# Kernel tuning notes

Measured on AMD Instinct MI355X. Metric: run time of the kernel, lower is better.

Reference implementation:

```python
import jax, jax.numpy as jnp
import numpy as np

N_FEATURES = 170
D_MODEL = 64
N_HEADS = 4
ALPHA = 0.1
LN_EPS = 1e-5
LEAKY_SLOPE = 0.01  # torch F.leaky_relu default
N = 3 * N_FEATURES  # 510
B = 32


def setup_inputs() -> dict:
    key = jax.random.key(0)
    ks = jax.random.split(key, 10)
    D, H = D_MODEL, N_HEADS
    s = 1.0 / np.sqrt(D)
    return {
        "x": jax.random.normal(ks[0], (B, N, D), dtype=jnp.float32),
        "causal_graph": jax.random.uniform(ks[1], (N, N), dtype=jnp.float32),
        # nn.Linear(d_model, d_model*n_heads, bias=False): stored here as (D, H*D) for x @ W
        "W": jax.random.uniform(ks[2], (D, H * D), jnp.float32, -s, s),
        "attention_w": jax.random.normal(ks[3], (H, 2 * D), dtype=jnp.float32),
        # Conv2d(2, n_heads, 3, padding=1): OIHW kernel
        "conv_w": jax.random.uniform(ks[4], (H, 2, 3, 3), jnp.float32, -1/np.sqrt(18), 1/np.sqrt(18)),
        "conv_b": jax.random.uniform(ks[5], (H,), jnp.float32, -1/np.sqrt(18), 1/np.sqrt(18)),
        # nn.Linear(d_model, 2*d_model): stored as (D, 2D)
        "fcg_w": jax.random.uniform(ks[6], (D, 2 * D), jnp.float32, -s, s),
        "fcg_b": jax.random.uniform(ks[7], (2 * D,), jnp.float32, -s, s),
        "ln_g": jnp.ones((D,), jnp.float32),
        "ln_b": jnp.zeros((D,), jnp.float32),
    }


def reference(x, causal_graph, W, attention_w, conv_w, conv_b, fcg_w, fcg_b, ln_g, ln_b):
    Bz, Nn, D = x.shape
    H = N_HEADS
    # shared projection: (B, N, H, D)
    xt = (x @ W).reshape(Bz, Nn, H, D)
    # GAT-style additive scores: concat-dot decomposed into two dot products
    w1, w2 = attention_w[:, :D], attention_w[:, D:]  # each (H, D)
    s_i = jnp.einsum('bnhd,hd->bhn', xt, w1)  # source term
    s_j = jnp.einsum('bnhd,hd->bhn', xt, w2)  # target term
    e = s_i[:, :, :, None] + s_j[:, :, None, :]  # (B, H, N, N)
    A_eva = jnp.where(e >= 0, e, LEAKY_SLOPE * e)  # leaky_relu
    # fuse mean attention with causal graph via 3x3 conv
    A_mean = A_eva.mean(axis=1)  # (B, N, N)
    causal = jnp.broadcast_to(causal_graph[None], (Bz, Nn, Nn))
    stacked = jnp.stack([A_mean, causal], axis=1)  # (B, 2, N, N)
    A_st = jax.lax.conv_general_dilated(
        stacked, conv_w, window_strides=(1, 1), padding=((1, 1), (1, 1)),
        dimension_numbers=('NCHW', 'OIHW', 'NCHW'))
    A_st = A_st + conv_b[None, :, None, None]  # (B, H, N, N)
    A = jax.nn.softmax(ALPHA * A_eva + (1.0 - ALPHA) * A_st, axis=-1)
    # multi-head aggregation then head-mean
    out = jnp.einsum('bhnm,bmhd->bnhd', A, xt).mean(axis=2)  # (B, N, D)
    # GLU
    g = out @ fcg_w + fcg_b  # (B, N, 2D)
    a, b = g[..., :D], g[..., D:]
    glu = a * jax.nn.sigmoid(b)
    # residual + layernorm
    y = glu + x
    mu = y.mean(axis=-1, keepdims=True)
    var = ((y - mu) ** 2).mean(axis=-1, keepdims=True)
    y = (y - mu) * jax.lax.rsqrt(var + LN_EPS) * ln_g + ln_b
    return y, A
```

## Files before the change

kernel.cpp:

```cpp
#include <hip/hip_runtime.h>

#define Bz 32
#define Nn 510
#define Dd 64
#define Hh 4
#define HD_ 256
#define Kpad 512
#define ALPHA_ 0.1f
#define LNEPS 1e-5f
#define SLOPE 0.01f
#define NEG_INF -3.0e38f

typedef __attribute__((ext_vector_type(8))) short short8;
typedef __attribute__((ext_vector_type(4))) float floatx4;

__device__ inline float wredsum(float v) {
  #pragma unroll
  for (int off = 32; off; off >>= 1) v += __shfl_xor(v, off, 64);
  return v;
}
__device__ inline float wredmax(float v) {
  #pragma unroll
  for (int off = 32; off; off >>= 1) v = fmaxf(v, __shfl_xor(v, off, 64));
  return v;
}
__device__ inline unsigned short f2bf(float f) {
  unsigned int u = __float_as_uint(f);
  unsigned int r = (u + 0x7fffu + ((u >> 16) & 1u)) >> 16;
  return (unsigned short)r;
}

__global__ __launch_bounds__(256) void k1_xt(const float* __restrict__ x,
                                             const float* __restrict__ W,
                                             const float* __restrict__ attw,
                                             unsigned short* __restrict__ xtT,
                                             float* __restrict__ si,
                                             float* __restrict__ sj) {
  __shared__ float Wl[64][68];
  __shared__ float xr[32][68];
  __shared__ unsigned short st[64 * 33];
  const int t = threadIdx.x;
  const int rt = blockIdx.x;
  const int b = blockIdx.y;
  const int ch = blockIdx.z;
  #pragma unroll
  for (int k = 0; k < 4; k++) {
    int f = t + k * 256;
    int kr = f >> 4;
    int c = (f & 15) * 4;
    *(float4*)&Wl[kr][c] = *(const float4*)&W[kr * HD_ + ch * 64 + c];
  }
  #pragma unroll
  for (int k = 0; k < 2; k++) {
    int f = t + k * 256;
    int r = f >> 4;
    int c = (f & 15) * 4;
    int row = rt * 32 + r;
    float4 v = make_float4(0.f, 0.f, 0.f, 0.f);
    if (row < Nn) v = *(const float4*)&x[(b * Nn + row) * Dd + c];
    *(float4*)&xr[r][c] = v;
  }
  __syncthreads();
  const int tg = t >> 4;
  const int tc = t & 15;
  const int rb = tg * 2, c0 = tc * 4;
  float acc[2][4] = {};
  #pragma unroll
  for (int k4 = 0; k4 < 16; k4++) {
    float4 xv0 = *(float4*)&xr[rb][k4 * 4];
    float4 xv1 = *(float4*)&xr[rb + 1][k4 * 4];
    #pragma unroll
    for (int kk = 0; kk < 4; kk++) {
      float4 wv = *(float4*)&Wl[k4 * 4 + kk][c0];
      float xs0 = (&xv0.x)[kk];
      float xs1 = (&xv1.x)[kk];
      acc[0][0] = fmaf(xs0, wv.x, acc[0][0]);
      acc[0][1] = fmaf(xs0, wv.y, acc[0][1]);
      acc[0][2] = fmaf(xs0, wv.z, acc[0][2]);
      acc[0][3] = fmaf(xs0, wv.w, acc[0][3]);
      acc[1][0] = fmaf(xs1, wv.x, acc[1][0]);
      acc[1][1] = fmaf(xs1, wv.y, acc[1][1]);
      acc[1][2] = fmaf(xs1, wv.z, acc[1][2]);
      acc[1][3] = fmaf(xs1, wv.w, acc[1][3]);
    }
  }
  #pragma unroll
  for (int cc = 0; cc < 4; cc++) {
    #pragma unroll
    for (int r = 0; r < 2; r++) {
      st[(c0 + cc) * 33 + rb + r] = f2bf(acc[r][cc]);
    }
  }
  float w1v[4], w2v[4];
  #pragma unroll
  for (int cc = 0; cc < 4; cc++) {
    w1v[cc] = attw[ch * 128 + c0 + cc];
    w2v[cc] = attw[ch * 128 + 64 + c0 + cc];
  }
  #pragma unroll
  for (int r = 0; r < 2; r++) {
    float p1 = acc[r][0] * w1v[0] + acc[r][1] * w1v[1] +
               acc[r][2] * w1v[2] + acc[r][3] * w1v[3];
    float p2 = acc[r][0] * w2v[0] + acc[r][1] * w2v[1] +
               acc[r][2] * w2v[2] + acc[r][3] * w2v[3];
    #pragma unroll
    for (int off = 1; off <= 8; off <<= 1) {
      p1 += __shfl_xor(p1, off, 64);
      p2 += __shfl_xor(p2, off, 64);
    }
    if (tc == 0) {
      int row = rt * 32 + rb + r;
      if (row < Nn) {
        si[(b * 4 + ch) * Nn + row] = p1;
        sj[(b * 4 + ch) * Nn + row] = p2;
      }
    }
  }
  __syncthreads();
  if (t < 64) {
    unsigned short* dst = &xtT[((size_t)(b * 4 + ch) * 64 + t) * Kpad + rt * 32];
    #pragma unroll
    for (int q = 0; q < 4; q++) {
      short8 v;
      #pragma unroll
      for (int k = 0; k < 8; k++) v[k] = (short)st[t * 33 + q * 8 + k];
      *(short8*)&dst[q * 8] = v;
    }
  }
}

__global__ __launch_bounds__(256) void k2a_cconv(const float* __restrict__ causal,
                                                 const float* __restrict__ convw,
                                                 const float* __restrict__ convb,
                                                 float* __restrict__ ccv) {
  const int i = blockIdx.x;
  const int t = threadIdx.x;
  #pragma unroll
  for (int qq = 0; qq < 2; qq++) {
    const int j = t + qq * 256;
    float tap[9];
    #pragma unroll
    for (int r3 = 0; r3 < 3; r3++) {
      int ii = i - 1 + r3;
      #pragma unroll
      for (int c3 = 0; c3 < 3; c3++) {
        int jj = j - 1 + c3;
        tap[r3 * 3 + c3] = (ii >= 0 && ii < Nn && jj >= 0 && jj < Nn)
                               ? causal[ii * Nn + jj] : 0.f;
      }
    }
    #pragma unroll
    for (int h = 0; h < 4; h++) {
      float acc = convb[h];
      #pragma unroll
      for (int q = 0; q < 9; q++) acc = fmaf(convw[h * 18 + 9 + q], tap[q], acc);
      ccv[((size_t)h * Nn + i) * 512 + j] = acc;
    }
  }
}

__global__ __launch_bounds__(256) void k2_attn(const float* __restrict__ si,
                                               const float* __restrict__ sj,
                                               const float* __restrict__ ccv,
                                               const float* __restrict__ convw,
                                               float* __restrict__ A) {
  __shared__ float am_t[10 * 8 * 68];
  __shared__ float sjl[4 * 8 * 68];
  __shared__ float sil[4][12];
  __shared__ float cwl[4][9];
  const int t = threadIdx.x;
  const int i0 = blockIdx.x * 8;
  const int b = blockIdx.y;
  if (t < 36) cwl[t / 9][t % 9] = convw[(t / 9) * 18 + (t % 9)];
  if (t < 40) {
    int h = t / 10, r = t % 10;
    int iq = i0 + r - 1;
    sil[h][r] = (iq >= 0 && iq < Nn) ? si[(b * 4 + h) * Nn + iq] : 0.f;
  }
  if (t >= 64 && t < 224) {
    int q = t - 64;
    int r = q >> 4, rem = q & 15;
    int e = rem >> 1, side = rem & 1;
    am_t[(r * 8 + e) * 68 + side * 65] = 0.f;
  }
  for (int f = t; f < 2048; f += 256) {
    int h = f >> 9, j = f & 511;
    float v = (j < Nn) ? sj[(b * 4 + h) * Nn + j] : 0.f;
    sjl[(h * 8 + (j & 7)) * 68 + (j >> 3) + 1] = v;
  }
  __syncthreads();
  for (int f = t; f < 5120; f += 256) {
    int r = f >> 9, j = f & 511;
    int iq = i0 + r - 1;
    float am = 0.f;
    if (iq >= 0 && iq < Nn && j < Nn) {
      float s = 0.f;
      #pragma unroll
      for (int h = 0; h < 4; h++) {
        float e2 = sil[h][r] + sjl[(h * 8 + (j & 7)) * 68 + (j >> 3) + 1];
        s += (e2 >= 0.f) ? e2 : SLOPE * e2;
      }
      am = 0.25f * s;
    }
    am_t[(r * 8 + (j & 7)) * 68 + (j >> 3) + 1] = am;
  }
  __syncthreads();
  const int w = t >> 6, L = t & 63;
  const int j0 = L * 8;
  #pragma unroll
  for (int qq = 0; qq < 2; qq++) {
    const int il = w * 2 + qq;
    const int i = i0 + il;
    if (i >= Nn) continue;
    float conv[4][8];
    #pragma unroll
    for (int h = 0; h < 4; h++) {
      const float* cp = &ccv[((size_t)h * Nn + i) * 512 + j0];
      float4 c0 = *(const float4*)&cp[0];
      float4 c1 = *(const float4*)&cp[4];
      conv[h][0] = c0.x; conv[h][1] = c0.y; conv[h][2] = c0.z; conv[h][3] = c0.w;
      conv[h][4] = c1.x; conv[h][5] = c1.y; conv[h][6] = c1.z; conv[h][7] = c1.w;
    }
    #pragma unroll
    for (int r3 = 0; r3 < 3; r3++) {
      const float* ba = &am_t[((il + r3) * 8) * 68];
      float a[10];
      a[0] = ba[7 * 68 + L];
      #pragma unroll
      for (int e = 0; e < 8; e++) a[1 + e] = ba[e * 68 + L + 1];
      a[9] = ba[0 * 68 + L + 2];
      #pragma unroll
      for (int h = 0; h < 4; h++) {
        float w0 = cwl[h][r3 * 3], w1 = cwl[h][r3 * 3 + 1], w2 = cwl[h][r3 * 3 + 2];
        #pragma unroll
        for (int e = 0; e < 8; e++) {
          float cv = conv[h][e];
          cv = fmaf(w0, a[e], cv);
          cv = fmaf(w1, a[e + 1], cv);
          cv = fmaf(w2, a[e + 2], cv);
          conv[h][e] = cv;
        }
      }
    }
    #pragma unroll
    for (int h = 0; h < 4; h++) {
      const float sih = sil[h][il + 1];
      float v[8];
      float mx = NEG_INF;
      #pragma unroll
      for (int e = 0; e < 8; e++) {
        float ee = sih + sjl[(h * 8 + e) * 68 + L + 1];
        float l = (ee >= 0.f) ? ee : SLOPE * ee;
        float val = ALPHA_ * l + (1.0f - ALPHA_) * conv[h][e];
        v[e] = (j0 + e < Nn) ? val : NEG_INF;
        mx = fmaxf(mx, v[e]);
      }
      mx = wredmax(mx);
      float p[8], s = 0.f;
      #pragma unroll
      for (int e = 0; e < 8; e++) {
        p[e] = __expf(v[e] - mx);
        s += p[e];
      }
      s = wredsum(s);
      const float inv = 1.f / s;
      #pragma unroll
      for (int e = 0; e < 8; e++) p[e] *= inv;
      float* Ar = &A[((size_t)(b * 4 + h) * Nn + i) * Nn + j0];
      *(float4*)&Ar[0] = make_float4(p[0], p[1], p[2], p[3]);
      if (L < 63) {
        *(float4*)&Ar[4] = make_float4(p[4], p[5], p[6], p[7]);
      } else {
        *(float2*)&Ar[4] = make_float2(p[4], p[5]);
      }
    }
  }
}

__global__ __launch_bounds__(256) void k3_out(const float* __restrict__ A,
                                              const unsigned short* __restrict__ xtT,
                                              const float* __restrict__ x,
                                              const float* __restrict__ fcgw,
                                              const float* __restrict__ fcgb,
                                              const float* __restrict__ lng,
                                              const float* __restrict__ lnb,
                                              float* __restrict__ y) {
  __shared__ unsigned short Asub[2][16 * 72];
  __shared__ float ol[16][64];
  __shared__ float gl[2][128];
  const int t = threadIdx.x;
  const int n0 = blockIdx.x * 16;
  const int b = blockIdx.y;
  const int w = t >> 6, L = t & 63;
  const int quad = L >> 4, l16 = L & 15;
  const int wc = w * 16;
  const int ar = t >> 4;
  const int amc = (t & 15) * 4;
  const int nrow = n0 + ar;
  floatx4 acc = {0.f, 0.f, 0.f, 0.f};

  auto stage = [&](int p) {
    const int h = p >> 3;
    const int m = (p & 7) * 64 + amc;
    float av[4] = {0.f, 0.f, 0.f, 0.f};
    if (nrow < Nn) {
      const float* src = &A[((size_t)(b * 4 + h) * Nn + nrow) * Nn + m];
      if (m + 3 < Nn) {
        float2 v0 = *(const float2*)&src[0];
        float2 v1 = *(const float2*)&src[2];
        av[0] = v0.x; av[1] = v0.y; av[2] = v1.x; av[3] = v1.y;
      } else {
        int lim = Nn - m;
        #pragma unroll
        for (int q = 0; q < 4; q++) if (q < lim) av[q] = src[q];
      }
    }
    ushort4 u;
    u.x = f2bf(av[0]); u.y = f2bf(av[1]);
    u.z = f2bf(av[2]); u.w = f2bf(av[3]);
    *(ushort4*)&Asub[p & 1][ar * 72 + amc] = u;
  };

  stage(0);
  __syncthreads();
  #pragma unroll 2
  for (int p = 0; p < 32; p++) {
    if (p + 1 < 32) stage(p + 1);
    const int h = p >> 3;
    const unsigned short* Xr =
        &xtT[((size_t)(b * 4 + h) * 64 + wc + l16) * Kpad + (p & 7) * 64];
    short8 af0 = *(short8*)&Asub[p & 1][l16 * 72 + quad * 8];
    short8 bf0 = *(const short8*)&Xr[quad * 8];
    acc = __builtin_amdgcn_mfma_f32_16x16x32_bf16(af0, bf0, acc, 0, 0, 0);
    short8 af1 = *(short8*)&Asub[p & 1][l16 * 72 + 32 + quad * 8];
    short8 bf1 = *(const short8*)&Xr[32 + quad * 8];
    acc = __builtin_amdgcn_mfma_f32_16x16x32_bf16(af1, bf1, acc, 0, 0, 0);
    __syncthreads();
  }

  #pragma unroll
  for (int reg = 0; reg < 4; reg++) {
    ol[quad * 4 + reg][wc + l16] = 0.25f * acc[reg];
  }
  __syncthreads();
  const int kk = t & 127;
  const int rg = t >> 7;
  for (int it = 0; it < 8; it++) {
    const int r = it * 2 + rg;
    const int row = n0 + r;
    float g = fcgb[kk];
    #pragma unroll
    for (int d = 0; d < 64; d++) g = fmaf(ol[r][d], fcgw[d * 128 + kk], g);
    gl[rg][kk] = g;
    __syncthreads();
    if (kk < 64 && row < Nn) {
      float a = gl[rg][kk];
      float bb = gl[rg][kk + 64];
      float glu = a / (1.f + __expf(-bb));
      float yv = glu + x[(b * Nn + row) * Dd + kk];
      float mu = wredsum(yv) * (1.f / 64.f);
      float dv = yv - mu;
      float var = wredsum(dv * dv) * (1.f / 64.f);
      float o = dv * rsqrtf(var + LNEPS) * lng[kk] + lnb[kk];
      y[(b * Nn + row) * Dd + kk] = o;
    }
    __syncthreads();
  }
}

extern "C" void kernel_launch(void* const* d_in, const int* in_sizes, int n_in,
                              void* d_out, int out_size, void* d_ws, size_t ws_size,
                              hipStream_t stream) {
  const float* x      = (const float*)d_in[0];
  const float* causal = (const float*)d_in[1];
  const float* W      = (const float*)d_in[2];
  const float* attw   = (const float*)d_in[3];
  const float* convw  = (const float*)d_in[4];
  const float* convb  = (const float*)d_in[5];
  const float* fcgw   = (const float*)d_in[6];
  const float* fcgb   = (const float*)d_in[7];
  const float* lng    = (const float*)d_in[8];
  const float* lnb    = (const float*)d_in[9];

  float* ws = (float*)d_ws;
  float* si = ws;
  float* sj = si + (size_t)Bz * Hh * Nn;
  unsigned short* xtT = (unsigned short*)(sj + (size_t)Bz * Hh * Nn + 16);
  float* ccv = (float*)(xtT + (size_t)Bz * Hh * Dd * Kpad);

  float* yout = (float*)d_out;
  float* Aout = yout + (size_t)Bz * Nn * Dd;

  k2a_cconv<<<dim3(Nn), 256, 0, stream>>>(causal, convw, convb, ccv);
  k1_xt  <<<dim3(16, Bz, 4), 256, 0, stream>>>(x, W, attw, xtT, si, sj);
  k2_attn<<<dim3(64, Bz), 256, 0, stream>>>(si, sj, ccv, convw, Aout);
  k3_out <<<dim3(32, Bz), 256, 0, stream>>>(Aout, xtT, x, fcgw, fcgb, lng, lnb, yout);
}
```

Before: 260.5 us.

## Compute attention-mean tile in registers with wave shuffles instead of LDS

The attention kernel no longer stages sj, si, conv weights and the mean-attention halo tile in shared memory behind two barriers. Each thread now loads its own sj and si values into registers and recomputes the leaky-relu head-mean for its three conv rows. Neighbouring columns for the 3x3 stencil come from wave shuffles. This removes LDS traffic and synchronisation, but adds redundant ALU work (mean rows recomputed per wave), more register pressure, and direct global reads of the conv weights.

```diff
diff --git a/kernel.cpp b/kernel.cpp
--- a/kernel.cpp
+++ b/kernel.cpp
@@ -164,94 +164,90 @@
                                                const float* __restrict__ ccv,
                                                const float* __restrict__ convw,
                                                float* __restrict__ A) {
-  __shared__ float am_t[10 * 8 * 68];
-  __shared__ float sjl[4 * 8 * 68];
-  __shared__ float sil[4][12];
-  __shared__ float cwl[4][9];
   const int t = threadIdx.x;
   const int i0 = blockIdx.x * 8;
   const int b = blockIdx.y;
-  if (t < 36) cwl[t / 9][t % 9] = convw[(t / 9) * 18 + (t % 9)];
-  if (t < 40) {
-    int h = t / 10, r = t % 10;
-    int iq = i0 + r - 1;
-    sil[h][r] = (iq >= 0 && iq < Nn) ? si[(b * 4 + h) * Nn + iq] : 0.f;
-  }
-  if (t >= 64 && t < 224) {
-    int q = t - 64;
-    int r = q >> 4, rem = q & 15;
-    int e = rem >> 1, side = rem & 1;
-    am_t[(r * 8 + e) * 68 + side * 65] = 0.f;
-  }
-  for (int f = t; f < 2048; f += 256) {
-    int h = f >> 9, j = f & 511;
-    float v = (j < Nn) ? sj[(b * 4 + h) * Nn + j] : 0.f;
-    sjl[(h * 8 + (j & 7)) * 68 + (j >> 3) + 1] = v;
-  }
-  __syncthreads();
-  for (int f = t; f < 5120; f += 256) {
-    int r = f >> 9, j = f & 511;
-    int iq = i0 + r - 1;
-    float am = 0.f;
-    if (iq >= 0 && iq < Nn && j < Nn) {
-      float s = 0.f;
-      #pragma unroll
-      for (int h = 0; h < 4; h++) {
-        float e2 = sil[h][r] + sjl[(h * 8 + (j & 7)) * 68 + (j >> 3) + 1];
-        s += (e2 >= 0.f) ? e2 : SLOPE * e2;
-      }
-      am = 0.25f * s;
-    }
-    am_t[(r * 8 + (j & 7)) * 68 + (j >> 3) + 1] = am;
-  }
-  __syncthreads();
   const int w = t >> 6, L = t & 63;
   const int j0 = L * 8;
+  float sjv[4][8];
+  #pragma unroll
+  for (int h = 0; h < 4; h++) {
+    const float* bp = &sj[(size_t)(b * 4 + h) * Nn];
+    if (j0 + 7 < Nn) {
+      #pragma unroll
+      for (int q = 0; q < 4; q++) {
+        float2 v = *(const float2*)&bp[j0 + q * 2];
+        sjv[h][q * 2] = v.x;
+        sjv[h][q * 2 + 1] = v.y;
+      }
+    } else {
+      #pragma unroll
+      for (int e = 0; e < 8; e++) sjv[h][e] = (j0 + e < Nn) ? bp[j0 + e] : 0.f;
+    }
+  }
+  float silr[4][4];
+  #pragma unroll
+  for (int rr = 0; rr < 4; rr++) {
+    int iq = i0 + w * 2 - 1 + rr;
+    bool ok = (iq >= 0 && iq < Nn);
+    #pragma unroll
+    for (int h = 0; h < 4; h++)
+      silr[h][rr] = ok ? si[(size_t)(b * 4 + h) * Nn + iq] : 0.f;
+  }
   #pragma unroll
   for (int qq = 0; qq < 2; qq++) {
-    const int il = w * 2 + qq;
-    const int i = i0 + il;
+    const int i = i0 + w * 2 + qq;
     if (i >= Nn) continue;
-    float conv[4][8];
+    float am[3][10];
+    #pragma unroll
+    for (int rr = 0; rr < 3; rr++) {
+      int iq = i - 1 + rr;
+      bool rowOK = (iq >= 0 && iq < Nn);
+      #pragma unroll
+      for (int e = 0; e < 8; e++) {
+        float s = 0.f;
+        #pragma unroll
+        for (int h = 0; h < 4; h++) {
+          float e2 = silr[h][qq + rr] + sjv[h][e];
+          s += (e2 >= 0.f) ? e2 : SLOPE * e2;
+        }
+        am[rr][1 + e] = (rowOK && (j0 + e < Nn)) ? 0.25f * s : 0.f;
+      }
+      float up = __shfl_up(am[rr][8], 1);
+      am[rr][0] = (L > 0) ? up : 0.f;
+      float dn = __shfl_down(am[rr][1], 1);
+      am[rr][9] = (L < 63) ? dn : 0.f;
+    }
     #pragma unroll
     for (int h = 0; h < 4; h++) {
       const float* cp = &ccv[((size_t)h * Nn + i) * 512 + j0];
       float4 c0 = *(const float4*)&cp[0];
       float4 c1 = *(const float4*)&cp[4];
-      conv[h][0] = c0.x; conv[h][1] = c0.y; conv[h][2] = c0.z; conv[h][3] = c0.w;
-      conv[h][4] = c1.x; conv[h][5] = c1.y; conv[h][6] = c1.z; conv[h][7] = c1.w;
-    }
-    #pragma unroll
-    for (int r3 = 0; r3 < 3; r3++) {
-      const float* ba = &am_t[((il + r3) * 8) * 68];
-      float a[10];
-      a[0] = ba[7 * 68 + L];
-      #pragma unroll
-      for (int e = 0; e < 8; e++) a[1 + e] = ba[e * 68 + L + 1];
-      a[9] = ba[0 * 68 + L + 2];
-      #pragma unroll
-      for (int h = 0; h < 4; h++) {
-        float w0 = cwl[h][r3 * 3], w1 = cwl[h][r3 * 3 + 1], w2 = cwl[h][r3 * 3 + 2];
+      float conv[8];
+      conv[0] = c0.x; conv[1] = c0.y; conv[2] = c0.z; conv[3] = c0.w;
+      conv[4] = c1.x; conv[5] = c1.y; conv[6] = c1.z; conv[7] = c1.w;
+      #pragma unroll
+      for (int r3 = 0; r3 < 3; r3++) {
+        float w0 = convw[h * 18 + r3 * 3];
+        float w1 = convw[h * 18 + r3 * 3 + 1];
+        float w2 = convw[h * 18 + r3 * 3 + 2];
         #pragma unroll
         for (int e = 0; e < 8; e++) {
-          float cv = conv[h][e];
-          cv = fmaf(w0, a[e], cv);
-          cv = fmaf(w1, a[e + 1], cv);
-          cv = fmaf(w2, a[e + 2], cv);
-          conv[h][e] = cv;
+          float cv = conv[e];
+          cv = fmaf(w0, am[r3][e], cv);
+          cv = fmaf(w1, am[r3][e + 1], cv);
+          cv = fmaf(w2, am[r3][e + 2], cv);
+          conv[e] = cv;
         }
       }
-    }
-    #pragma unroll
-    for (int h = 0; h < 4; h++) {
-      const float sih = sil[h][il + 1];
+      const float sih = silr[h][qq + 1];
       float v[8];
       float mx = NEG_INF;
       #pragma unroll
       for (int e = 0; e < 8; e++) {
-        float ee = sih + sjl[(h * 8 + e) * 68 + L + 1];
+        float ee = sih + sjv[h][e];
         float l = (ee >= 0.f) ? ee : SLOPE * ee;
-        float val = ALPHA_ * l + (1.0f - ALPHA_) * conv[h][e];
+        float val = ALPHA_ * l + (1.0f - ALPHA_) * conv[e];
         v[e] = (j0 + e < Nn) ? val : NEG_INF;
         mx = fmaxf(mx, v[e]);
       }
```

Result: slower. 276.7 us (+6.2%).
